# Optimization experiments

Measured on AMD Instinct MI355X. Metric: run time of the kernel, lower is better.

The kernel has to match this reference:

```python
import jax, jax.numpy as jnp
import numpy as np
from jax import lax

BN_EPS = 1e-4  # both BatchNorm2d (epsilon=0.0001) and BatchNorm1d (eps=0.0001)


def bin_act(x):
    # deterministic 1-bit activation: 2*round(clamp((x+1)/2,0,1)) - 1
    return 2.0 * jnp.round(jnp.clip((x + 1.0) * 0.5, 0.0, 1.0)) - 1.0


def bin_w(w):
    # H = 1.0: wb = (round(clamp((w+1)/2,0,1))*2 - 1) * 1.0  -> values in {-1,+1}
    return 2.0 * jnp.round(jnp.clip((w + 1.0) * 0.5, 0.0, 1.0)) - 1.0


def conv3x3(x, w, b):
    # NCHW input, OIHW weight, stride 1, padding 1 (SAME for 3x3)
    y = lax.conv_general_dilated(x, bin_w(w), (1, 1), ((1, 1), (1, 1)),
                                 dimension_numbers=('NCHW', 'OIHW', 'NCHW'))
    return y + b[None, :, None, None]


def maxpool2(x):
    return lax.reduce_window(x, -jnp.inf, lax.max, (1, 1, 2, 2), (1, 1, 2, 2), 'VALID')


def bn2d(x, g, b):
    # training-mode BatchNorm2d: batch stats over (N,H,W), biased variance
    m = jnp.mean(x, axis=(0, 2, 3), keepdims=True)
    v = jnp.mean(jnp.square(x - m), axis=(0, 2, 3), keepdims=True)
    return (x - m) * lax.rsqrt(v + BN_EPS) * g[None, :, None, None] + b[None, :, None, None]


def bn1d(x, g, b):
    m = jnp.mean(x, axis=0)
    v = jnp.mean(jnp.square(x - m), axis=0)
    return (x - m) * lax.rsqrt(v + BN_EPS) * g + b


def linear(x, w, b):
    return x @ bin_w(w).T + b


def setup_inputs() -> dict:
    key = jax.random.key(0)
    ks = jax.random.split(key, 16)
    d = {}
    d['x'] = jax.random.normal(ks[0], (256, 3, 32, 32), jnp.float32)
    conv_shapes = [(128, 3), (128, 128), (256, 128), (256, 256), (512, 256), (512, 512)]
    for i, (co, ci) in enumerate(conv_shapes, start=1):
        d[f'cw{i}'] = jax.random.normal(ks[i], (co, ci, 3, 3), jnp.float32)
        d[f'cb{i}'] = jax.random.normal(jax.random.fold_in(ks[i], 1), (co,), jnp.float32) * 0.01
        d[f'g{i}'] = jnp.ones((co,), jnp.float32)
        d[f'be{i}'] = jnp.zeros((co,), jnp.float32)
    fc_shapes = [(1024, 8192), (1024, 1024), (10, 1024)]
    for i, (fo, fi) in enumerate(fc_shapes, start=1):
        d[f'fw{i}'] = jax.random.normal(ks[6 + i], (fo, fi), jnp.float32)
        d[f'fb{i}'] = jax.random.normal(jax.random.fold_in(ks[6 + i], 1), (fo,), jnp.float32) * 0.01
        d[f'gf{i}'] = jnp.ones((fo,), jnp.float32)
        d[f'bef{i}'] = jnp.zeros((fo,), jnp.float32)
    return d


def reference(x, cw1, cb1, g1, be1, cw2, cb2, g2, be2, cw3, cb3, g3, be3,
              cw4, cb4, g4, be4, cw5, cb5, g5, be5, cw6, cb6, g6, be6,
              fw1, fb1, gf1, bef1, fw2, fb2, gf2, bef2, fw3, fb3, gf3, bef3):
    x = bin_act(bn2d(conv3x3(x, cw1, cb1), g1, be1))                 # [B,128,32,32]
    x = bin_act(bn2d(maxpool2(conv3x3(x, cw2, cb2)), g2, be2))       # [B,128,16,16]
    x = bin_act(bn2d(conv3x3(x, cw3, cb3), g3, be3))                 # [B,256,16,16]
    x = bin_act(bn2d(maxpool2(conv3x3(x, cw4, cb4)), g4, be4))       # [B,256,8,8]
    x = bin_act(bn2d(conv3x3(x, cw5, cb5), g5, be5))                 # [B,512,8,8]
    x = bin_act(bn2d(maxpool2(conv3x3(x, cw6, cb6)), g6, be6))       # [B,512,4,4]
    x = x.reshape(x.shape[0], -1)                                     # [B,8192]
    x = bin_act(bn1d(linear(x, fw1, fb1), gf1, bef1))                 # [B,1024]
    x = bin_act(bn1d(linear(x, fw2, fb2), gf2, bef2))                 # [B,1024]
    x = bn1d(linear(x, fw3, fb3), gf3, bef3)                          # [B,10]
    return x
```

## Files before the change

kernel.cpp:

```cpp
#include <hip/hip_runtime.h>

using u64 = unsigned long long;


__device__ __forceinline__ int bin01(float x) {
  float u = (x + 1.0f) * 0.5f;
  u = fminf(fmaxf(u, 0.0f), 1.0f);
  return rintf(u) != 0.0f;
}

__global__ void pack_conv_w(const float* __restrict__ w, u64* __restrict__ out,
                            int Cout, int Cin) {
  const int cqn = Cin >> 6;
  const int total = Cout * 9 * cqn;
  const int idx = blockIdx.x * 256 + threadIdx.x;
  if (idx >= total) return;
  int r = idx;
  const int q = r % cqn; r /= cqn;
  const int kx = r % 3; r /= 3;
  const int ky = r % 3;
  const int co = r / 3;
  u64 word = 0;
  for (int l = 0; l < 64; ++l) {
    const int ci = q * 64 + l;
    if (bin01(w[((size_t)(co * Cin + ci) * 3 + ky) * 3 + kx])) word |= (1ull << l);
  }
  out[idx] = word;
}

__global__ void pack_fc_w(const float* __restrict__ w, u64* __restrict__ out,
                          int Fi, int Fo) {
  const int fiq = Fi >> 6;
  const int total = Fo * fiq;
  const int idx = blockIdx.x * 256 + threadIdx.x;
  if (idx >= total) return;
  const int q = idx % fiq, o = idx / fiq;
  u64 word = 0;
  for (int l = 0; l < 64; ++l)
    if (bin01(w[(size_t)o * Fi + q * 64 + l])) word |= (1ull << l);
  out[idx] = word;
}

__global__ void pack_fc1_w(const float* __restrict__ w, u64* __restrict__ out) {
  const int idx = blockIdx.x * 256 + threadIdx.x;
  const int o = idx >> 7, q = idx & 127;
  const int hw = q >> 3, cq = q & 7;
  u64 word = 0;
  for (int l = 0; l < 64; ++l) {
    const int f = (cq * 64 + l) * 16 + hw;
    if (bin01(w[(size_t)o * 8192 + f])) word |= (1ull << l);
  }
  out[idx] = word;
}

__global__ void pack_w1f(const float* __restrict__ w1, float* __restrict__ w1f) {
  const int i = blockIdx.x * 256 + threadIdx.x;
  if (i < 3456) w1f[i] = bin01(w1[i]) ? 1.0f : -1.0f;
}

__device__ __forceinline__ void stage_image(const float* __restrict__ x, int n,
                                            float* __restrict__ xs, int nthreads,
                                            int t) {
  for (int idx = t; idx < 3 * 34 * 34; idx += nthreads) {
    const int ci = idx / 1156, rem = idx % 1156;
    const int hy = rem / 34, wx = rem % 34;
    float v = 0.0f;
    if (hy >= 1 && hy <= 32 && wx >= 1 && wx <= 32)
      v = x[(size_t)n * 3072 + ci * 1024 + (hy - 1) * 32 + (wx - 1)];
    xs[idx] = v;
  }
}

template <int PASS>
__global__ void conv1_eval(const float* __restrict__ x,
                           const float* __restrict__ w1f,
                           const float* __restrict__ cb,
                           const float* __restrict__ st,
                           float* __restrict__ BL) {
  const int blk = blockIdx.x;
  const int n = blk >> 2, q = blk & 3;
  const int t = threadIdx.x;
  __shared__ float xs[3 * 34 * 34];
  __shared__ float yl[256 * 8];
  __shared__ float rl[2 * 8 * 8];
  stage_image(x, n, xs, 256, t);
  __syncthreads();
  const int hw = q * 256 + t;
  const int h = hw >> 5, w = hw & 31;
  float win[27];
#pragma unroll
  for (int k = 0; k < 27; ++k) {
    const int ci = k / 9, dy = (k % 9) / 3, dx = k % 3;
    win[k] = xs[ci * 1156 + (h + dy) * 34 + (w + dx)];
  }
  for (int cc = 0; cc < 16; ++cc) {
    float y8[8];
#pragma unroll
    for (int j8 = 0; j8 < 8; ++j8) {
      const int c = cc * 8 + j8;
      const float* wp = w1f + c * 27;
      float acc = 0.0f;
#pragma unroll
      for (int k = 0; k < 27; ++k) acc = fmaf(wp[k], win[k], acc);
      float y = acc + cb[c];
      if (PASS) { const float d = y - st[2 * c]; y = d * d; }
      y8[j8] = y;
    }
    __syncthreads();
#pragma unroll
    for (int j8 = 0; j8 < 8; ++j8) yl[t * 8 + j8] = y8[j8];
    __syncthreads();
    if (t < 128) {
      const int L = t >> 6, j = (t >> 3) & 7, c8 = t & 7;
      float r = yl[(L * 128 + j) * 8 + c8];
      for (int i = 1; i < 16; ++i) r += yl[(L * 128 + i * 8 + j) * 8 + c8];
      rl[(L * 8 + c8) * 8 + j] = r;
    }
    __syncthreads();
    if (t < 16) {
      const int L = t >> 3, c8 = t & 7;
      const float* p = rl + (L * 8 + c8) * 8;
      const float s =
          ((p[0] + p[1]) + (p[2] + p[3])) + ((p[4] + p[5]) + (p[6] + p[7]));
      BL[((size_t)(n * 8) + (q * 2 + L)) * 128 + (cc * 8 + c8)] = s;
    }
  }
}

__global__ void conv1_comb2(const float* __restrict__ BL, float* __restrict__ st,
                            int pass) {
  const int t = threadIdx.x;
  const int lane = t & 63;
  const int wid = t >> 6;
  const int c = blockIdx.x * 32 + wid * 8 + (lane & 7);
  const int leaf = lane >> 3;
  const float* base = BL + (size_t)leaf * 128 + c;
  float S = 0.0f;
#pragma unroll 4
  for (int n = 0; n < 256; ++n) {
    const float v = base[(size_t)n * 1024];
    const float a = v + __shfl_xor(v, 8);
    const float b = a + __shfl_xor(a, 16);
    const float Ln = b + __shfl_xor(b, 32);
    S = (n == 0) ? Ln : (S + Ln);
  }
  if (leaf == 0) {
    if (pass == 0) st[2 * c] = S / 262144.0f;
    else           st[2 * c + 1] = 1.0f / sqrtf(S / 262144.0f + 1e-4f);
  }
}

__global__ void conv1_binz(const float* __restrict__ x,
                           const float* __restrict__ w1f,
                           const float* __restrict__ cb,
                           const float* __restrict__ st,
                           const float* __restrict__ g,
                           const float* __restrict__ be,
                           u64* __restrict__ out) {
  const int blk = blockIdx.x;
  const int n = blk >> 2, q = blk & 3;
  const int t = threadIdx.x;
  __shared__ float xs[3 * 34 * 34];
  stage_image(x, n, xs, 256, t);
  __syncthreads();
  const int hw = q * 256 + t;
  const int h = hw >> 5, w = hw & 31;
  float win[27];
#pragma unroll
  for (int k = 0; k < 27; ++k) {
    const int ci = k / 9, dy = (k % 9) / 3, dx = k % 3;
    win[k] = xs[ci * 1156 + (h + dy) * 34 + (w + dx)];
  }
  u64 m0 = 0, m1 = 0;
  for (int c = 0; c < 128; ++c) {
    const float* wp = w1f + c * 27;
    float acc = 0.0f;
#pragma unroll
    for (int k = 0; k < 27; ++k) acc = fmaf(wp[k], win[k], acc);
    const float y = acc + cb[c];
    const float tv = ((y - st[2 * c]) * st[2 * c + 1]) * g[c] + be[c];
    const u64 bit = (u64)bin01(tv);
    if (c < 64) m0 |= bit << c;
    else        m1 |= bit << (c - 64);
  }
  u64* dst = out + ((size_t)(n * 1024 + hw)) * 2;
  dst[0] = m0;
  dst[1] = m1;
}

template <int CQ, int POOL, int H, int COUT, int NCPB>
__launch_bounds__(256, 4)
__global__ void conv_bin(const u64* __restrict__ xin, const u64* __restrict__ wpk,
                         short* __restrict__ pre) {
  constexpr int OH = H / POOL;
  constexpr int PLANE = OH * OH;
  constexpr int G = 256 / PLANE;
  constexpr int NE = POOL * POOL;
  constexpr int NW_ = H * H * CQ;
  constexpr int QC = (CQ > 4) ? 4 : CQ;
  constexpr int NQC = CQ / QC;
  const int n = blockIdx.x;
  const int t = threadIdx.x;
  __shared__ u64 xs[NW_];
  const u64* src = xin + (size_t)n * NW_;
  for (int i = t; i < NW_; i += 256) xs[i] = src[i];
  __syncthreads();
  const int cosub = t / PLANE;
  const int pos = t % PLANE;
  const int oh = pos / OH, ow = pos % OH;

  int pc[NCPB][NE];
#pragma unroll
  for (int cc = 0; cc < NCPB; ++cc)
#pragma unroll
    for (int e = 0; e < NE; ++e) pc[cc][e] = 0;

#pragma unroll
  for (int qc = 0; qc < NQC; ++qc) {
#pragma unroll
    for (int k = 0; k < 9; ++k) {
      const int dy = k / 3, dx = k % 3;
      u64 cw[NE][QC];
      bool cv[NE];
#pragma unroll
      for (int py = 0; py < POOL; ++py) {
#pragma unroll
        for (int px = 0; px < POOL; ++px) {
          const int hh = oh * POOL + py + dy - 1;
          const int ww = ow * POOL + px + dx - 1;
          const bool v = ((unsigned)hh < (unsigned)H) && ((unsigned)ww < (unsigned)H);
          const int e = py * POOL + px;
          cv[e] = v;
          const int base = v ? ((hh * H + ww) * CQ + qc * QC) : 0;
#pragma unroll
          for (int q = 0; q < QC; ++q) cw[e][q] = xs[base + q];
        }
      }
#pragma unroll
      for (int cc = 0; cc < NCPB; ++cc) {
        const int co = (blockIdx.y * NCPB + cc) * G + cosub;
        const u64* wp = wpk + ((size_t)co * 9 + k) * CQ + qc * QC;
        u64 w[QC];
#pragma unroll
        for (int q = 0; q < QC; ++q) w[q] = wp[q];
#pragma unroll
        for (int e = 0; e < NE; ++e) {
          int tp = 0;
#pragma unroll
          for (int q = 0; q < QC; ++q) tp += __popcll(cw[e][q] ^ w[q]);
          pc[cc][e] += cv[e] ? tp : 0;
        }
      }
    }
  }

  int vcnt[NE];
#pragma unroll
  for (int py = 0; py < POOL; ++py) {
#pragma unroll
    for (int px = 0; px < POOL; ++px) {
      int cvn = 0;
#pragma unroll
      for (int dy = 0; dy < 3; ++dy)
#pragma unroll
        for (int dx = 0; dx < 3; ++dx) {
          const int hh = oh * POOL + py + dy - 1, ww = ow * POOL + px + dx - 1;
          cvn += (((unsigned)hh < (unsigned)H) && ((unsigned)ww < (unsigned)H)) ? 1 : 0;
        }
      vcnt[py * POOL + px] = cvn;
    }
  }
#pragma unroll
  for (int cc = 0; cc < NCPB; ++cc) {
    const int co = (blockIdx.y * NCPB + cc) * G + cosub;
    int best = -1000000;
#pragma unroll
    for (int e = 0; e < NE; ++e) {
      const int dot = vcnt[e] * (CQ * 64) - 2 * pc[cc][e];
      best = dot > best ? dot : best;
    }
    pre[((size_t)(n * COUT + co) * OH + oh) * OH + ow] = (short)best;
  }
}

template <int PASS>
__device__ __forceinline__ float acc8(const short* __restrict__ p, float b, float m,
                                      int start, int len) {
  float r[8];
#pragma unroll
  for (int j = 0; j < 8; ++j) {
    float y = (float)p[start + j] + b;
    if (PASS) { const float d = y - m; y = d * d; }
    r[j] = y;
  }
  for (int i = 8; i < len; i += 8) {
#pragma unroll
    for (int j = 0; j < 8; ++j) {
      float y = (float)p[start + i + j] + b;
      if (PASS) { const float d = y - m; y = d * d; }
      r[j] += y;
    }
  }
  return ((r[0] + r[1]) + (r[2] + r[3])) + ((r[4] + r[5]) + (r[6] + r[7]));
}

template <int PASS>
__device__ __forceinline__ float np_sum_hw(const short* __restrict__ p, float b,
                                           float m, int HW) {
  if (HW == 256) return acc8<PASS>(p, b, m, 0, 128) + acc8<PASS>(p, b, m, 128, 128);
  return acc8<PASS>(p, b, m, 0, HW);
}

template <int HW>
__global__ void conv_stats(const short* __restrict__ pre, const float* __restrict__ cb,
                           float* __restrict__ st, int Cout) {
  const int c = blockIdx.x;
  const int n = threadIdx.x;
  const float b = cb[c];
  const short* p = pre + ((size_t)n * Cout + c) * HW;
  __shared__ float ls[256];
  ls[n] = np_sum_hw<0>(p, b, 0.0f, HW);
  __syncthreads();
  __shared__ float ms;
  if (n == 0) {
    float S = ls[0];
    for (int i = 1; i < 256; ++i) S += ls[i];
    ms = S / (float)(256 * HW);
  }
  __syncthreads();
  const float m = ms;
  __syncthreads();
  ls[n] = np_sum_hw<1>(p, b, m, HW);
  __syncthreads();
  if (n == 0) {
    float S = ls[0];
    for (int i = 1; i < 256; ++i) S += ls[i];
    const float v = S / (float)(256 * HW);
    st[2 * c] = m;
    st[2 * c + 1] = 1.0f / sqrtf(v + 1e-4f);
  }
}

__global__ void bin2d(const short* __restrict__ pre, const float* __restrict__ st,
                      const float* __restrict__ cb, const float* __restrict__ g,
                      const float* __restrict__ be, u64* __restrict__ out,
                      int Cout, int OH) {
  const int CQ = Cout >> 6;
  const int HW = OH * OH;
  const int widx = blockIdx.x * 256 + threadIdx.x;
  const int hw = widx % HW;
  const int r = widx / HW;
  const int cq = r % CQ;
  const int n = r / CQ;
  const short* p = pre + ((size_t)(n * Cout + cq * 64)) * HW + hw;
  u64 mask = 0;
  for (int c = 0; c < 64; ++c) {
    const int ch = cq * 64 + c;
    const float val = (float)p[(size_t)c * HW] + cb[ch];
    const float tv = ((val - st[2 * ch]) * st[2 * ch + 1]) * g[ch] + be[ch];
    mask |= ((u64)bin01(tv)) << c;
  }
  out[((size_t)n * HW + hw) * CQ + cq] = mask;
}

__global__ void fc_layer(const u64* __restrict__ xin, const u64* __restrict__ wpk,
                         short* __restrict__ pre, int FiQ, int Fo) {
  const int o = blockIdx.x;
  const int n = threadIdx.x;
  const u64* xp = xin + (size_t)n * FiQ;
  const u64* wp = wpk + (size_t)o * FiQ;
  int pc = 0;
  for (int q = 0; q < FiQ; ++q) pc += __popcll(xp[q] ^ wp[q]);
  pre[(size_t)n * Fo + o] = (short)(FiQ * 64 - 2 * pc);
}

__global__ void fc_stats(const short* __restrict__ pre, const float* __restrict__ fb,
                         float* __restrict__ st, int Fo) {
  const int o = blockIdx.x * blockDim.x + threadIdx.x;
  if (o >= Fo) return;
  const float b = fb[o];
  float S = (float)pre[o] + b;
#pragma unroll 8
  for (int n = 1; n < 256; ++n) S += (float)pre[(size_t)n * Fo + o] + b;
  const float m = S / 256.0f;
  float d0 = (float)pre[o] + b - m;
  float V = d0 * d0;
#pragma unroll 8
  for (int n = 1; n < 256; ++n) {
    const float d = (float)pre[(size_t)n * Fo + o] + b - m;
    V += d * d;
  }
  st[2 * o] = m;
  st[2 * o + 1] = 1.0f / sqrtf(V / 256.0f + 1e-4f);
}

__global__ void fc_bin(const short* __restrict__ pre, const float* __restrict__ st,
                       const float* __restrict__ fb, const float* __restrict__ g,
                       const float* __restrict__ be, u64* __restrict__ out, int Fo) {
  const int gid = blockIdx.x * 4 + (threadIdx.x >> 6);
  const int lane = threadIdx.x & 63;
  const int OQ = Fo >> 6;
  const int oq = gid % OQ, n = gid / OQ;
  const int o = oq * 64 + lane;
  const float val = (float)pre[(size_t)n * Fo + o] + fb[o];
  const float tv = ((val - st[2 * o]) * st[2 * o + 1]) * g[o] + be[o];
  const u64 mask = __ballot(bin01(tv));
  if (lane == 0) out[(size_t)n * OQ + oq] = mask;
}

__global__ void fc_out(const short* __restrict__ pre, const float* __restrict__ st,
                       const float* __restrict__ fb, const float* __restrict__ g,
                       const float* __restrict__ be, float* __restrict__ out) {
  const int i = blockIdx.x * 256 + threadIdx.x;
  if (i >= 2560) return;
  const int o = i % 10;
  const float val = (float)pre[i] + fb[o];
  out[i] = ((val - st[2 * o]) * st[2 * o + 1]) * g[o] + be[o];
}

extern "C" void kernel_launch(void* const* d_in, const int* in_sizes, int n_in,
                              void* d_out, int out_size, void* d_ws, size_t ws_size,
                              hipStream_t stream) {
  if (n_in < 37) return;
  const float* x = (const float*)d_in[0];
  const float *cw1 = (const float*)d_in[1],  *cb1 = (const float*)d_in[2],  *g1 = (const float*)d_in[3],  *be1 = (const float*)d_in[4];
  const float *cw2 = (const float*)d_in[5],  *cb2 = (const float*)d_in[6],  *g2 = (const float*)d_in[7],  *be2 = (const float*)d_in[8];
  const float *cw3 = (const float*)d_in[9],  *cb3 = (const float*)d_in[10], *g3 = (const float*)d_in[11], *be3 = (const float*)d_in[12];
  const float *cw4 = (const float*)d_in[13], *cb4 = (const float*)d_in[14], *g4 = (const float*)d_in[15], *be4 = (const float*)d_in[16];
  const float *cw5 = (const float*)d_in[17], *cb5 = (const float*)d_in[18], *g5 = (const float*)d_in[19], *be5 = (const float*)d_in[20];
  const float *cw6 = (const float*)d_in[21], *cb6 = (const float*)d_in[22], *g6 = (const float*)d_in[23], *be6 = (const float*)d_in[24];
  const float *fw1 = (const float*)d_in[25], *fb1 = (const float*)d_in[26], *gf1 = (const float*)d_in[27], *bef1 = (const float*)d_in[28];
  const float *fw2 = (const float*)d_in[29], *fb2 = (const float*)d_in[30], *gf2 = (const float*)d_in[31], *bef2 = (const float*)d_in[32];
  const float *fw3 = (const float*)d_in[33], *fb3 = (const float*)d_in[34], *gf3 = (const float*)d_in[35], *bef3 = (const float*)d_in[36];
  float* out = (float*)d_out;

  char* ws = (char*)d_ws;
  if (ws_size < 46137344) return;
  float* ST = (float*)ws;
  float* W1F = (float*)(ws + 32768);
  float* BL = (float*)(ws + 65536);
  u64* W = (u64*)(ws + 1179648);
  u64* A = (u64*)(ws + 2981888);
  short* PRE = (short*)(ws + 12582912);
  const int S1 = 0, S2 = 256, S3 = 512, S4 = 1024, S5 = 1536, S6 = 2560;
  const int SF1 = 3584, SF2 = 5632, SF3 = 7680;
  const size_t WC2 = 0, WC3 = 2304, WC4 = 6912, WC5 = 16128, WC6 = 34560;
  const size_t WF1 = 71424, WF2 = 202496, WF3 = 218880;
  const size_t A1 = 0, A2 = 524288, A3 = 655360, A4 = 917504, A5 = 983040;
  const size_t A6 = 1114112, AF1 = 1146880, AF2 = 1150976;

  pack_w1f<<<14, 256, 0, stream>>>(cw1, W1F);
  pack_conv_w<<<9, 256, 0, stream>>>(cw2, W + WC2, 128, 128);
  pack_conv_w<<<18, 256, 0, stream>>>(cw3, W + WC3, 256, 128);
  pack_conv_w<<<36, 256, 0, stream>>>(cw4, W + WC4, 256, 256);
  pack_conv_w<<<72, 256, 0, stream>>>(cw5, W + WC5, 512, 256);
  pack_conv_w<<<144, 256, 0, stream>>>(cw6, W + WC6, 512, 512);
  pack_fc1_w<<<512, 256, 0, stream>>>(fw1, W + WF1);
  pack_fc_w<<<64, 256, 0, stream>>>(fw2, W + WF2, 1024, 1024);
  pack_fc_w<<<1, 256, 0, stream>>>(fw3, W + WF3, 1024, 10);

  conv1_eval<0><<<1024, 256, 0, stream>>>(x, W1F, cb1, ST + S1, BL);
  conv1_comb2<<<4, 256, 0, stream>>>(BL, ST + S1, 0);
  conv1_eval<1><<<1024, 256, 0, stream>>>(x, W1F, cb1, ST + S1, BL);
  conv1_comb2<<<4, 256, 0, stream>>>(BL, ST + S1, 1);
  conv1_binz<<<1024, 256, 0, stream>>>(x, W1F, cb1, ST + S1, g1, be1, A + A1);

  conv_bin<2, 2, 32, 128, 8><<<dim3(256, 16), 256, 0, stream>>>(A + A1, W + WC2, PRE);
  conv_stats<256><<<128, 256, 0, stream>>>(PRE, cb2, ST + S2, 128);
  bin2d<<<512, 256, 0, stream>>>(PRE, ST + S2, cb2, g2, be2, A + A2, 128, 16);

  conv_bin<2, 1, 16, 256, 8><<<dim3(256, 32), 256, 0, stream>>>(A + A2, W + WC3, PRE);
  conv_stats<256><<<256, 256, 0, stream>>>(PRE, cb3, ST + S3, 256);
  bin2d<<<1024, 256, 0, stream>>>(PRE, ST + S3, cb3, g3, be3, A + A3, 256, 16);

  conv_bin<4, 2, 16, 256, 4><<<dim3(256, 16), 256, 0, stream>>>(A + A3, W + WC4, PRE);
  conv_stats<64><<<256, 256, 0, stream>>>(PRE, cb4, ST + S4, 256);
  bin2d<<<256, 256, 0, stream>>>(PRE, ST + S4, cb4, g4, be4, A + A4, 256, 8);

  conv_bin<4, 1, 8, 512, 8><<<dim3(256, 16), 256, 0, stream>>>(A + A4, W + WC5, PRE);
  conv_stats<64><<<512, 256, 0, stream>>>(PRE, cb5, ST + S5, 512);
  bin2d<<<512, 256, 0, stream>>>(PRE, ST + S5, cb5, g5, be5, A + A5, 512, 8);

  conv_bin<8, 2, 8, 512, 4><<<dim3(256, 8), 256, 0, stream>>>(A + A5, W + WC6, PRE);
  conv_stats<16><<<512, 256, 0, stream>>>(PRE, cb6, ST + S6, 512);
  bin2d<<<128, 256, 0, stream>>>(PRE, ST + S6, cb6, g6, be6, A + A6, 512, 4);

  fc_layer<<<1024, 256, 0, stream>>>(A + A6, W + WF1, PRE, 128, 1024);
  fc_stats<<<16, 64, 0, stream>>>(PRE, fb1, ST + SF1, 1024);
  fc_bin<<<1024, 256, 0, stream>>>(PRE, ST + SF1, fb1, gf1, bef1, A + AF1, 1024);

  fc_layer<<<1024, 256, 0, stream>>>(A + AF1, W + WF2, PRE, 16, 1024);
  fc_stats<<<16, 64, 0, stream>>>(PRE, fb2, ST + SF2, 1024);
  fc_bin<<<1024, 256, 0, stream>>>(PRE, ST + SF2, fb2, gf2, bef2, A + AF2, 1024);

  fc_layer<<<10, 256, 0, stream>>>(A + AF2, W + WF3, PRE, 16, 10);
  fc_stats<<<1, 64, 0, stream>>>(PRE, fb3, ST + SF3, 10);
  fc_out<<<10, 256, 0, stream>>>(PRE, ST + SF3, fb3, gf3, bef3, out);
}
```

Baseline: 1.158 ms.

## Zero-pad activations in shared memory and correct border popcounts via precomputed table

The binary conv kernel now stages a zero-padded activation tile in shared memory, so the inner loop drops per-tap bounds checks and validity masks. Padded taps XOR to the weight bits, so a new kernel precomputes, per output channel and border class, the weight popcount over the out-of-image taps, and the epilogue subtracts it. This simplifies the hot popcount loop and address arithmetic at the cost of a larger shared tile, an extra small kernel launch, and a table lookup in the epilogue. cosub is also made wave-uniform with readfirstlane when the plane spans a full wave.

```diff
diff --git a/kernel.cpp b/kernel.cpp
--- a/kernel.cpp
+++ b/kernel.cpp
@@ -26,6 +26,32 @@
     if (bin01(w[((size_t)(co * Cin + ci) * 3 + ky) * 3 + kx])) word |= (1ull << l);
   }
   out[idx] = word;
+}
+
+__global__ void pack_corr(const u64* __restrict__ W, int* __restrict__ CT) {
+  const int idx = blockIdx.x * 256 + threadIdx.x;
+  const int b1 = 1152, b2 = 3456, b3 = 5760, b4 = 10368, b5 = 14976;
+  if (idx >= b5) return;
+  int lo, woff, cq;
+  if (idx < b1)      { lo = 0;  woff = 0;     cq = 2; }
+  else if (idx < b2) { lo = b1; woff = 2304;  cq = 2; }
+  else if (idx < b3) { lo = b2; woff = 6912;  cq = 4; }
+  else if (idx < b4) { lo = b3; woff = 16128; cq = 4; }
+  else               { lo = b4; woff = 34560; cq = 8; }
+  const int rel = idx - lo;
+  const int co = rel / 9, p = rel % 9;
+  const int r = p / 3, c = p % 3;
+  int corr = 0;
+  for (int dy = 0; dy < 3; ++dy)
+    for (int dx = 0; dx < 3; ++dx) {
+      const bool inv = (r == 1 && dy == 0) || (r == 2 && dy == 2) ||
+                       (c == 1 && dx == 0) || (c == 2 && dx == 2);
+      if (inv) {
+        const u64* wp = W + woff + ((size_t)(co * 9 + dy * 3 + dx)) * cq;
+        for (int q = 0; q < cq; ++q) corr += __popcll(wp[q]);
+      }
+    }
+  CT[idx] = corr;
 }
 
 __global__ void pack_fc_w(const float* __restrict__ w, u64* __restrict__ out,
@@ -191,24 +217,43 @@
 template <int CQ, int POOL, int H, int COUT, int NCPB>
 __launch_bounds__(256, 4)
 __global__ void conv_bin(const u64* __restrict__ xin, const u64* __restrict__ wpk,
-                         short* __restrict__ pre) {
+                         const int* __restrict__ ct, short* __restrict__ pre) {
   constexpr int OH = H / POOL;
   constexpr int PLANE = OH * OH;
   constexpr int G = 256 / PLANE;
   constexpr int NE = POOL * POOL;
-  constexpr int NW_ = H * H * CQ;
+  constexpr int HP = H + 2;
+  constexpr int NWP = HP * HP * CQ;
   constexpr int QC = (CQ > 4) ? 4 : CQ;
   constexpr int NQC = CQ / QC;
   const int n = blockIdx.x;
   const int t = threadIdx.x;
-  __shared__ u64 xs[NW_];
-  const u64* src = xin + (size_t)n * NW_;
-  for (int i = t; i < NW_; i += 256) xs[i] = src[i];
-  __syncthreads();
-  const int cosub = t / PLANE;
+  __shared__ u64 xs[NWP];
+  const u64* src = xin + (size_t)n * (H * H * CQ);
+  for (int i = t; i < NWP; i += 256) {
+    const int q = i & (CQ - 1);
+    const int rem = i / CQ;
+    const int wx = rem % HP;
+    const int hy = rem / HP;
+    u64 v = 0;
+    if ((unsigned)(hy - 1) < (unsigned)H && (unsigned)(wx - 1) < (unsigned)H)
+      v = src[((hy - 1) * H + (wx - 1)) * CQ + q];
+    xs[i] = v;
+  }
+  __syncthreads();
+  int cosub;
+  if constexpr (PLANE >= 64) cosub = __builtin_amdgcn_readfirstlane(t / PLANE);
+  else cosub = t / PLANE;
   const int pos = t % PLANE;
   const int oh = pos / OH, ow = pos % OH;
 
+  int cbase[NE];
+#pragma unroll
+  for (int py = 0; py < POOL; ++py)
+#pragma unroll
+    for (int px = 0; px < POOL; ++px)
+      cbase[py * POOL + px] = ((oh * POOL + py) * HP + (ow * POOL + px)) * CQ;
+
   int pc[NCPB][NE];
 #pragma unroll
   for (int cc = 0; cc < NCPB; ++cc)
@@ -220,21 +265,13 @@
 #pragma unroll
     for (int k = 0; k < 9; ++k) {
       const int dy = k / 3, dx = k % 3;
+      const int koff = (dy * HP + dx) * CQ + qc * QC;
       u64 cw[NE][QC];
-      bool cv[NE];
-#pragma unroll
-      for (int py = 0; py < POOL; ++py) {
-#pragma unroll
-        for (int px = 0; px < POOL; ++px) {
-          const int hh = oh * POOL + py + dy - 1;
-          const int ww = ow * POOL + px + dx - 1;
-          const bool v = ((unsigned)hh < (unsigned)H) && ((unsigned)ww < (unsigned)H);
-          const int e = py * POOL + px;
-          cv[e] = v;
-          const int base = v ? ((hh * H + ww) * CQ + qc * QC) : 0;
-#pragma unroll
-          for (int q = 0; q < QC; ++q) cw[e][q] = xs[base + q];
-        }
+#pragma unroll
+      for (int e = 0; e < NE; ++e) {
+        const u64* cp = &xs[cbase[e] + koff];
+#pragma unroll
+        for (int q = 0; q < QC; ++q) cw[e][q] = cp[q];
       }
 #pragma unroll
       for (int cc = 0; cc < NCPB; ++cc) {
@@ -245,10 +282,10 @@
         for (int q = 0; q < QC; ++q) w[q] = wp[q];
 #pragma unroll
         for (int e = 0; e < NE; ++e) {
-          int tp = 0;
-#pragma unroll
-          for (int q = 0; q < QC; ++q) tp += __popcll(cw[e][q] ^ w[q]);
-          pc[cc][e] += cv[e] ? tp : 0;
+          int acc = pc[cc][e];
+#pragma unroll
+          for (int q = 0; q < QC; ++q) acc += __popcll(cw[e][q] ^ w[q]);
+          pc[cc][e] = acc;
         }
       }
     }
@@ -270,13 +307,24 @@
       vcnt[py * POOL + px] = cvn;
     }
   }
+  int cofs[NE];
+#pragma unroll
+  for (int py = 0; py < POOL; ++py)
+#pragma unroll
+    for (int px = 0; px < POOL; ++px) {
+      const int chh = oh * POOL + py, cww = ow * POOL + px;
+      const int rr = (chh == 0) ? 1 : ((chh == H - 1) ? 2 : 0);
+      const int cl = (cww == 0) ? 1 : ((cww == H - 1) ? 2 : 0);
+      cofs[py * POOL + px] = rr * 3 + cl;
+    }
 #pragma unroll
   for (int cc = 0; cc < NCPB; ++cc) {
     const int co = (blockIdx.y * NCPB + cc) * G + cosub;
+    const int* ctp = ct + co * 9;
     int best = -1000000;
 #pragma unroll
     for (int e = 0; e < NE; ++e) {
-      const int dot = vcnt[e] * (CQ * 64) - 2 * pc[cc][e];
+      const int dot = vcnt[e] * (CQ * 64) - 2 * (pc[cc][e] - ctp[cofs[e]]);
       best = dot > best ? dot : best;
     }
     pre[((size_t)(n * COUT + co) * OH + oh) * OH + ow] = (short)best;
@@ -441,6 +489,7 @@
   float* BL = (float*)(ws + 65536);
   u64* W = (u64*)(ws + 1179648);
   u64* A = (u64*)(ws + 2981888);
+  int* CT = (int*)(ws + 12222464);
   short* PRE = (short*)(ws + 12582912);
   const int S1 = 0, S2 = 256, S3 = 512, S4 = 1024, S5 = 1536, S6 = 2560;
   const int SF1 = 3584, SF2 = 5632, SF3 = 7680;
@@ -448,6 +497,7 @@
   const size_t WF1 = 71424, WF2 = 202496, WF3 = 218880;
   const size_t A1 = 0, A2 = 524288, A3 = 655360, A4 = 917504, A5 = 983040;
   const size_t A6 = 1114112, AF1 = 1146880, AF2 = 1150976;
+  const int CT2 = 0, CT3 = 1152, CT4 = 3456, CT5 = 5760, CT6 = 10368;
 
   pack_w1f<<<14, 256, 0, stream>>>(cw1, W1F);
   pack_conv_w<<<9, 256, 0, stream>>>(cw2, W + WC2, 128, 128);
@@ -455,6 +505,7 @@
   pack_conv_w<<<36, 256, 0, stream>>>(cw4, W + WC4, 256, 256);
   pack_conv_w<<<72, 256, 0, stream>>>(cw5, W + WC5, 512, 256);
   pack_conv_w<<<144, 256, 0, stream>>>(cw6, W + WC6, 512, 512);
+  pack_corr<<<59, 256, 0, stream>>>(W, CT);
   pack_fc1_w<<<512, 256, 0, stream>>>(fw1, W + WF1);
   pack_fc_w<<<64, 256, 0, stream>>>(fw2, W + WF2, 1024, 1024);
   pack_fc_w<<<1, 256, 0, stream>>>(fw3, W + WF3, 1024, 10);
@@ -465,23 +516,23 @@
   conv1_comb2<<<4, 256, 0, stream>>>(BL, ST + S1, 1);
   conv1_binz<<<1024, 256, 0, stream>>>(x, W1F, cb1, ST + S1, g1, be1, A + A1);
 
-  conv_bin<2, 2, 32, 128, 8><<<dim3(256, 16), 256, 0, stream>>>(A + A1, W + WC2, PRE);
+  conv_bin<2, 2, 32, 128, 8><<<dim3(256, 16), 256, 0, stream>>>(A + A1, W + WC2, CT + CT2, PRE);
   conv_stats<256><<<128, 256, 0, stream>>>(PRE, cb2, ST + S2, 128);
   bin2d<<<512, 256, 0, stream>>>(PRE, ST + S2, cb2, g2, be2, A + A2, 128, 16);
 
-  conv_bin<2, 1, 16, 256, 8><<<dim3(256, 32), 256, 0, stream>>>(A + A2, W + WC3, PRE);
+  conv_bin<2, 1, 16, 256, 8><<<dim3(256, 32), 256, 0, stream>>>(A + A2, W + WC3, CT + CT3, PRE);
   conv_stats<256><<<256, 256, 0, stream>>>(PRE, cb3, ST + S3, 256);
   bin2d<<<1024, 256, 0, stream>>>(PRE, ST + S3, cb3, g3, be3, A + A3, 256, 16);
 
-  conv_bin<4, 2, 16, 256, 4><<<dim3(256, 16), 256, 0, stream>>>(A + A3, W + WC4, PRE);
+  conv_bin<4, 2, 16, 256, 4><<<dim3(256, 16), 256, 0, stream>>>(A + A3, W + WC4, CT + CT4, PRE);
   conv_stats<64><<<256, 256, 0, stream>>>(PRE, cb4, ST + S4, 256);
   bin2d<<<256, 256, 0, stream>>>(PRE, ST + S4, cb4, g4, be4, A + A4, 256, 8);
 
-  conv_bin<4, 1, 8, 512, 8><<<dim3(256, 16), 256, 0, stream>>>(A + A4, W + WC5, PRE);
+  conv_bin<4, 1, 8, 512, 8><<<dim3(256, 16), 256, 0, stream>>>(A + A4, W + WC5, CT + CT5, PRE);
   conv_stats<64><<<512, 256, 0, stream>>>(PRE, cb5, ST + S5, 512);
   bin2d<<<512, 256, 0, stream>>>(PRE, ST + S5, cb5, g5, be5, A + A5, 512, 8);
 
-  conv_bin<8, 2, 8, 512, 4><<<dim3(256, 8), 256, 0, stream>>>(A + A5, W + WC6, PRE);
+  conv_bin<8, 2, 8, 512, 4><<<dim3(256, 8), 256, 0, stream>>>(A + A5, W + WC6, CT + CT6, PRE);
   conv_stats<16><<<512, 256, 0, stream>>>(PRE, cb6, ST + S6, 512);
   bin2d<<<128, 256, 0, stream>>>(PRE, ST + S6, cb6, g6, be6, A + A6, 512, 4);
 
```

New measurement: 1.377 ms. 1.19x slower.
